# Kernel tuning notes

Measured on AMD Instinct MI355X. Metric: run time of the kernel, lower is better.

The kernel has to match this reference:

```python
import jax, jax.numpy as jnp
import numpy as np


def _l2n(v, eps=1e-12):
    return v / (jnp.linalg.norm(v) + eps)


def _sn(W, u):
    # Spectral normalization with one power-iteration step.
    # W: [Cin, Cout] (1x1 conv kernel flattened), u: [Cin] persistent vector.
    v = _l2n(W.T @ u)            # [Cout]
    u_new = _l2n(W @ v)          # [Cin]
    v = jax.lax.stop_gradient(v)
    u_new = jax.lax.stop_gradient(u_new)
    sigma = u_new @ (W @ v)      # scalar, grads flow through W only
    return W / sigma


def _conv1x1(x, W, b, u):
    # x: [B,H,W,Cin], spectrally-normalized 1x1 conv == GEMM over channels
    return jnp.einsum('bhwc,cd->bhwd', x, _sn(W, u)) + b


def setup_inputs() -> dict:
    key = jax.random.key(0)
    ks = jax.random.split(key, 14)
    B, H, W, C = 8, 64, 64, 256
    Cq = C // 8  # 32
    s = lambda fan_in: 1.0 / np.sqrt(fan_in)
    return {
        'x':  jax.random.normal(ks[0], (B, H, W, C), jnp.float32),
        'Wf': jax.random.normal(ks[1], (C, Cq), jnp.float32) * s(C),
        'bf': jnp.zeros((Cq,), jnp.float32),
        'uf': jax.random.normal(ks[2], (C,), jnp.float32),
        'Wg': jax.random.normal(ks[3], (C, Cq), jnp.float32) * s(C),
        'bg': jnp.zeros((Cq,), jnp.float32),
        'ug': jax.random.normal(ks[4], (C,), jnp.float32),
        'Wh': jax.random.normal(ks[5], (C, C), jnp.float32) * s(C),
        'bh': jnp.zeros((C,), jnp.float32),
        'uh': jax.random.normal(ks[6], (C,), jnp.float32),
        'Wc': jax.random.normal(ks[7], (C, C), jnp.float32) * s(C),
        'bc': jnp.zeros((C,), jnp.float32),
        'uc': jax.random.normal(ks[8], (C,), jnp.float32),
        'gamma': jnp.float32(0.7),  # nonzero so attention branch contributes
    }


def reference(x, Wf, bf, uf, Wg, bg, ug, Wh, bh, uh, Wc, bc, uc, gamma):
    B, H, W, C = x.shape
    N = H * W
    flat = lambda t: t.reshape(B, N, t.shape[-1])
    f = flat(_conv1x1(x, Wf, bf, uf))   # [B,N,C/8] keys
    g = flat(_conv1x1(x, Wg, bg, ug))   # [B,N,C/8] queries
    h = flat(_conv1x1(x, Wh, bh, uh))   # [B,N,C]   values
    s = jnp.einsum('bqd,bkd->bqk', g, f)          # [B,N,N]
    beta = jax.nn.softmax(s, axis=-1)
    o = jnp.einsum('bqk,bkc->bqc', beta, h)       # [B,N,C]
    o = o.reshape(B, H, W, C)
    o = _conv1x1(o, Wc, bc, uc)
    return gamma * o + x
```

## Files before the change

kernel.cpp:

```cpp
#include <hip/hip_runtime.h>

typedef unsigned short ushort_t;
typedef __attribute__((ext_vector_type(8))) __bf16 bf16x8;
typedef __attribute__((ext_vector_type(4))) float f32x4;
typedef __attribute__((ext_vector_type(4))) ushort_t ushort4_t;

__device__ inline ushort_t f2bf(float f){
  __bf16 h = (__bf16)f;
  union { __bf16 h; ushort_t u; } v; v.h = h;
  return v.u;
}

__device__ inline f32x4 mfma16(bf16x8 a, bf16x8 b, f32x4 c){
  return __builtin_amdgcn_mfma_f32_16x16x32_bf16(a, b, c, 0, 0, 0);
}

#define GLDS16(gsrc, ldst) \
  __builtin_amdgcn_global_load_lds((const __attribute__((address_space(1))) unsigned int*)(gsrc), \
                                   (__attribute__((address_space(3))) unsigned int*)(ldst), 16, 0, 0)

__global__ void sigma_kernel(const float* __restrict__ Wf, const float* __restrict__ uf,
                             const float* __restrict__ Wg, const float* __restrict__ ug,
                             const float* __restrict__ Wh, const float* __restrict__ uh,
                             const float* __restrict__ Wc, const float* __restrict__ uc,
                             float* __restrict__ inv_sigma){
  int w = blockIdx.x, t = threadIdx.x;
  const float *W, *u; int Cout;
  if      (w == 0){ W = Wf; u = uf; Cout = 32; }
  else if (w == 1){ W = Wg; u = ug; Cout = 32; }
  else if (w == 2){ W = Wh; u = uh; Cout = 256; }
  else            { W = Wc; u = uc; Cout = 256; }
  __shared__ float su[256], sv[256], red[256];
  su[t] = u[t];
  __syncthreads();
  float v = 0.f;
  if (t < Cout){
    for (int i = 0; i < 256; ++i) v += W[i*Cout + t] * su[i];
  }
  red[t] = (t < Cout) ? v*v : 0.f;
  __syncthreads();
  for (int s = 128; s > 0; s >>= 1){ if (t < s) red[t] += red[t+s]; __syncthreads(); }
  float nv = sqrtf(red[0]) + 1e-12f;
  __syncthreads();
  if (t < Cout) sv[t] = v / nv;
  __syncthreads();
  float wv = 0.f;
  for (int d = 0; d < Cout; ++d) wv += W[t*Cout + d] * sv[d];
  __syncthreads();
  red[t] = wv * wv;
  __syncthreads();
  for (int s = 128; s > 0; s >>= 1){ if (t < s) red[t] += red[t+s]; __syncthreads(); }
  if (t == 0){
    float ss2 = red[0];
    float sig = ss2 / (sqrtf(ss2) + 1e-12f);
    inv_sigma[w] = 1.0f / sig;
  }
}

__global__ void prep_weights(const float* __restrict__ Wf, const float* __restrict__ Wg,
                             const float* __restrict__ Wh, const float* __restrict__ Wc,
                             const float* __restrict__ inv_sigma,
                             ushort_t* __restrict__ WallT, ushort_t* __restrict__ WcT){
  int idx = blockIdx.x * 256 + threadIdx.x;
  if (idx < 81920){
    int c = idx >> 8, k = idx & 255;
    float val, is;
    if (c < 32)      { val = Wf[k*32  + c      ]; is = inv_sigma[0]; }
    else if (c < 64) { val = Wg[k*32  + (c-32) ]; is = inv_sigma[1]; }
    else             { val = Wh[k*256 + (c-64) ]; is = inv_sigma[2]; }
    WallT[idx] = f2bf(val * is);
  } else {
    int j = idx - 81920; int c = j >> 8, k = j & 255;
    WcT[j] = f2bf(Wc[k*256 + c] * inv_sigma[3]);
  }
}

__global__ __launch_bounds__(256) void fgh_kernel(
    const float* __restrict__ x, const ushort_t* __restrict__ WallT,
    const float* __restrict__ bf, const float* __restrict__ bg, const float* __restrict__ bh,
    ushort_t* __restrict__ fO, ushort_t* __restrict__ gO, ushort_t* __restrict__ hT){
  __shared__ __attribute__((aligned(16))) char ldsX[4][16384];
  int t = threadIdx.x;
  int wv = t >> 6, l = t & 63, lrow = l & 15, lgrp = l >> 4;
  long r0 = (long)blockIdx.x * 64 + wv * 16;
  char* ldsW = ldsX[wv];
#pragma unroll
  for (int rloc = 0; rloc < 16; ++rloc){
    const char* src = (const char*)(x + (r0 + rloc)*256)
                    + ((l*16) ^ ((rloc & 7) << 4));
    GLDS16(src, ldsW + rloc*1024);
  }
  asm volatile("s_waitcnt vmcnt(0)" ::: "memory");
  const char* xrow = ldsW + lrow*1024;
  int swzX = (lrow & 7) << 4;
  f32x4 acc[20];
#pragma unroll
  for (int i = 0; i < 20; ++i) acc[i] = f32x4{0.f,0.f,0.f,0.f};
#pragma unroll
  for (int ks = 0; ks < 8; ++ks){
    int bb = ks*128 + lgrp*32;
    f32x4 xa = *(const f32x4*)(xrow + ( bb       ^ swzX));
    f32x4 xb = *(const f32x4*)(xrow + ((bb + 16) ^ swzX));
    union { __bf16 h[8]; bf16x8 v; } A;
#pragma unroll
    for (int j = 0; j < 4; ++j){ A.h[j] = (__bf16)xa[j]; A.h[4+j] = (__bf16)xb[j]; }
    int kk = ks*32 + lgrp*8;
#pragma unroll
    for (int ct = 0; ct < 20; ++ct){
      bf16x8 bbv = *(const bf16x8*)(WallT + (ct*16 + lrow)*256 + kk);
      acc[ct] = mfma16(A.v, bbv, acc[ct]);
    }
  }
#pragma unroll
  for (int ct = 0; ct < 20; ++ct){
    int col = ct*16 + lrow;
    long rowb = r0 + lgrp*4;
    if (col < 32){
      float bv = bf[col];
#pragma unroll
      for (int rg = 0; rg < 4; ++rg) fO[(rowb+rg)*32 + col] = f2bf(acc[ct][rg] + bv);
    } else if (col < 64){
      float bv = bg[col-32];
#pragma unroll
      for (int rg = 0; rg < 4; ++rg)
        gO[(rowb+rg)*32 + (col-32)] = f2bf((acc[ct][rg] + bv) * 1.44269504f);
    } else {
      int hc = col - 64;
      float bv = bh[hc];
      long bb2 = rowb >> 12, n = rowb & 4095;
      int k6 = (int)(n & 63);
      int s6 = (k6 & 32) | (((k6 >> 2) & 3) << 3) | (((k6 >> 4) & 1) << 2) | (k6 & 3);
      long pos = (n & ~63L) | (long)s6;
      ushort4_t pk;
#pragma unroll
      for (int rg = 0; rg < 4; ++rg) pk[rg] = f2bf(acc[ct][rg] + bv);
      *(ushort4_t*)(hT + (bb2*256 + hc)*4096 + pos) = pk;
    }
  }
}

__global__ __launch_bounds__(256, 2) void attn_kernel(
    const ushort_t* __restrict__ fI, const ushort_t* __restrict__ gI,
    const ushort_t* __restrict__ hT,
    ushort_t* __restrict__ oP, float* __restrict__ mP, float* __restrict__ liP){
  __shared__ ushort_t ldsV[256*64];
  int bid = blockIdx.x, t = threadIdx.x;
  int b = bid & 7, rest = bid >> 3, qt = rest >> 1, kh = rest & 1;
  int wv = t >> 6, l = t & 63, lrow = l & 15, lgrp = l >> 4;
  int q0 = qt*128 + wv*32;
  long key_base = (long)kh * 2048;
  const ushort_t* gB = gI + ((long)b*4096 + q0)*32;
  bf16x8 qa0 = *(const bf16x8*)(gB + lrow*32 + lgrp*8);
  bf16x8 qa1 = *(const bf16x8*)(gB + (16 + lrow)*32 + lgrp*8);
  const ushort_t* hB = hT + (long)b*256*4096;
  const ushort_t* kp = fI + (long)b*4096*32 + key_base*32 + lrow*32 + lgrp*8;
  const ushort_t* vsrc = hB + (long)(wv*64 + (l>>3))*4096 + key_base
                            + (((l & 7) ^ (l >> 3)) << 3);
  ushort_t* vdst = ldsV + wv*4096;
  f32x4 o0[16], o1[16];
#pragma unroll
  for (int i = 0; i < 16; ++i){ o0[i] = f32x4{0.f,0.f,0.f,0.f}; o1[i] = f32x4{0.f,0.f,0.f,0.f}; }
  float m0 = -1e30f, m1 = -1e30f, li0 = 0.f, li1 = 0.f;
  int swzR = (lrow & 7) << 3;
  for (int kt = 0; kt < 32; ++kt){
    __syncthreads();
    bf16x8 kb0 = *(const bf16x8*)(kp);
    bf16x8 kb1 = *(const bf16x8*)(kp + 512);
    bf16x8 kb2 = *(const bf16x8*)(kp + 1024);
    bf16x8 kb3 = *(const bf16x8*)(kp + 1536);
    kp += 2048;
    const ushort_t* vs = vsrc + kt*64;
#pragma unroll
    for (int i = 0; i < 8; ++i)
      GLDS16(vs + i*32768, vdst + i*512);
    f32x4 s00 = mfma16(kb0, qa0, f32x4{0.f,0.f,0.f,0.f});
    f32x4 s01 = mfma16(kb1, qa0, f32x4{0.f,0.f,0.f,0.f});
    f32x4 s02 = mfma16(kb2, qa0, f32x4{0.f,0.f,0.f,0.f});
    f32x4 s03 = mfma16(kb3, qa0, f32x4{0.f,0.f,0.f,0.f});
    f32x4 s10 = mfma16(kb0, qa1, f32x4{0.f,0.f,0.f,0.f});
    f32x4 s11 = mfma16(kb1, qa1, f32x4{0.f,0.f,0.f,0.f});
    f32x4 s12 = mfma16(kb2, qa1, f32x4{0.f,0.f,0.f,0.f});
    f32x4 s13 = mfma16(kb3, qa1, f32x4{0.f,0.f,0.f,0.f});
    float tm0 = -1e30f, tm1 = -1e30f;
#pragma unroll
    for (int rg = 0; rg < 4; ++rg){
      tm0 = fmaxf(tm0, fmaxf(fmaxf(s00[rg], s01[rg]), fmaxf(s02[rg], s03[rg])));
      tm1 = fmaxf(tm1, fmaxf(fmaxf(s10[rg], s11[rg]), fmaxf(s12[rg], s13[rg])));
    }
    tm0 = fmaxf(tm0, __shfl_xor(tm0, 16)); tm0 = fmaxf(tm0, __shfl_xor(tm0, 32));
    tm1 = fmaxf(tm1, __shfl_xor(tm1, 16)); tm1 = fmaxf(tm1, __shfl_xor(tm1, 32));
    if (__any((tm0 > m0 + 8.f) || (tm1 > m1 + 8.f))){
      float mn0 = fmaxf(m0, tm0), mn1 = fmaxf(m1, tm1);
      float sc0 = exp2f(m0 - mn0), sc1 = exp2f(m1 - mn1);
      m0 = mn0; m1 = mn1; li0 *= sc0; li1 *= sc1;
#pragma unroll
      for (int ct = 0; ct < 16; ++ct)
#pragma unroll
        for (int rg = 0; rg < 4; ++rg){ o0[ct][rg] *= sc0; o1[ct][rg] *= sc1; }
    }
    union { __bf16 h[8]; bf16x8 v; } pf00, pf01, pf10, pf11;
#pragma unroll
    for (int rg = 0; rg < 4; ++rg){
      float a0 = exp2f(s00[rg] - m0), a1 = exp2f(s01[rg] - m0);
      float a2 = exp2f(s02[rg] - m0), a3 = exp2f(s03[rg] - m0);
      li0 += (a0 + a1) + (a2 + a3);
      pf00.h[rg] = (__bf16)a0; pf00.h[4+rg] = (__bf16)a1;
      pf01.h[rg] = (__bf16)a2; pf01.h[4+rg] = (__bf16)a3;
      float c0 = exp2f(s10[rg] - m1), c1 = exp2f(s11[rg] - m1);
      float c2 = exp2f(s12[rg] - m1), c3 = exp2f(s13[rg] - m1);
      li1 += (c0 + c1) + (c2 + c3);
      pf10.h[rg] = (__bf16)c0; pf10.h[4+rg] = (__bf16)c1;
      pf11.h[rg] = (__bf16)c2; pf11.h[4+rg] = (__bf16)c3;
    }
    asm volatile("s_waitcnt vmcnt(0)" ::: "memory");
    __syncthreads();
    __builtin_amdgcn_s_setprio(1);
#pragma unroll
    for (int ct = 0; ct < 16; ++ct){
      int base = (ct*16 + lrow) << 6;
      bf16x8 vb0 = *(const bf16x8*)(ldsV + base + (( (lgrp << 3))      ^ swzR));
      bf16x8 vb1 = *(const bf16x8*)(ldsV + base + ((32 + (lgrp << 3)) ^ swzR));
      o0[ct] = mfma16(vb0, pf00.v, o0[ct]);
      o0[ct] = mfma16(vb1, pf01.v, o0[ct]);
      o1[ct] = mfma16(vb0, pf10.v, o1[ct]);
      o1[ct] = mfma16(vb1, pf11.v, o1[ct]);
    }
    __builtin_amdgcn_s_setprio(0);
  }
  li0 += __shfl_xor(li0, 16); li0 += __shfl_xor(li0, 32);
  li1 += __shfl_xor(li1, 16); li1 += __shfl_xor(li1, 32);
  long rbase = (long)b*4096 + q0;
  ushort_t* Ob = oP + ((long)kh*32768 + rbase)*256;
#pragma unroll
  for (int ct = 0; ct < 16; ++ct){
    ushort4_t pk0, pk1;
#pragma unroll
    for (int rg = 0; rg < 4; ++rg){ pk0[rg] = f2bf(o0[ct][rg]); pk1[rg] = f2bf(o1[ct][rg]); }
    *(ushort4_t*)(Ob + (long)lrow*256      + ct*16 + lgrp*4) = pk0;
    *(ushort4_t*)(Ob + (long)(16+lrow)*256 + ct*16 + lgrp*4) = pk1;
  }
  if (l < 16){
    mP [kh*32768 + rbase + lrow]      = m0;
    liP[kh*32768 + rbase + lrow]      = li0;
    mP [kh*32768 + rbase + 16 + lrow] = m1;
    liP[kh*32768 + rbase + 16 + lrow] = li1;
  }
}

__global__ __launch_bounds__(256) void out_kernel(
    const ushort_t* __restrict__ oP, const float* __restrict__ mP,
    const float* __restrict__ liP, const ushort_t* __restrict__ WcT,
    const float* __restrict__ bc, const float* __restrict__ x,
    const float* __restrict__ gamma, float* __restrict__ out){
  __shared__ __attribute__((aligned(16))) char ldsO[4][16384];
  int t = threadIdx.x;
  int wv = t >> 6, l = t & 63, lrow = l & 15, lgrp = l >> 4;
  long r0 = (long)blockIdx.x * 64 + wv * 16;
  char* ldsW = ldsO[wv];
#pragma unroll
  for (int i = 0; i < 8; ++i){
    int rloc = 2*i + (l >> 5);
    int soff = ((l & 31)*16) ^ ((rloc & 7) << 4);
    GLDS16((const char*)(oP + (r0 + rloc)*256) + soff,            ldsW + i*1024);
    GLDS16((const char*)(oP + (32768L + r0 + rloc)*256) + soff,   ldsW + 8192 + i*1024);
  }
  long r = r0 + lrow;
  float m1 = mP[r],  m2 = mP[32768 + r];
  float li1 = liP[r], li2 = liP[32768 + r];
  float mm  = fmaxf(m1, m2);
  float sc1 = exp2f(m1 - mm), sc2 = exp2f(m2 - mm);
  float inv = 1.0f / (li1*sc1 + li2*sc2);
  float w1 = sc1 * inv, w2 = sc2 * inv;
  asm volatile("s_waitcnt vmcnt(0)" ::: "memory");
  const char* orow = ldsW + lrow*512;
  int swzO = (lrow & 7) << 4;
  f32x4 acc[16];
#pragma unroll
  for (int i = 0; i < 16; ++i) acc[i] = f32x4{0.f,0.f,0.f,0.f};
#pragma unroll
  for (int ks = 0; ks < 8; ++ks){
    int bb = (ks*64 + lgrp*16) ^ swzO;
    bf16x8 a1 = *(const bf16x8*)(orow + bb);
    bf16x8 a2 = *(const bf16x8*)(orow + 8192 + bb);
    union { __bf16 h[8]; bf16x8 v; } A;
#pragma unroll
    for (int j = 0; j < 8; ++j)
      A.h[j] = (__bf16)((float)a1[j]*w1 + (float)a2[j]*w2);
    int kk = ks*32 + lgrp*8;
#pragma unroll
    for (int ct = 0; ct < 16; ++ct){
      bf16x8 bbv = *(const bf16x8*)(WcT + (ct*16 + lrow)*256 + kk);
      acc[ct] = mfma16(A.v, bbv, acc[ct]);
    }
  }
  float gm = gamma[0];
#pragma unroll
  for (int ct = 0; ct < 16; ++ct){
    int col = ct*16 + lrow;
    float bv = bc[col];
#pragma unroll
    for (int rg = 0; rg < 4; ++rg){
      long row = r0 + lgrp*4 + rg;
      out[row*256 + col] = gm*(acc[ct][rg] + bv) + x[row*256 + col];
    }
  }
}

extern "C" void kernel_launch(void* const* d_in, const int* in_sizes, int n_in,
                              void* d_out, int out_size, void* d_ws, size_t ws_size,
                              hipStream_t stream){
  (void)in_sizes; (void)n_in; (void)out_size; (void)ws_size;
  const float* x  = (const float*)d_in[0];
  const float* Wf = (const float*)d_in[1];
  const float* bf = (const float*)d_in[2];
  const float* uf = (const float*)d_in[3];
  const float* Wg = (const float*)d_in[4];
  const float* bg = (const float*)d_in[5];
  const float* ug = (const float*)d_in[6];
  const float* Wh = (const float*)d_in[7];
  const float* bh = (const float*)d_in[8];
  const float* uh = (const float*)d_in[9];
  const float* Wc = (const float*)d_in[10];
  const float* bc = (const float*)d_in[11];
  const float* uc = (const float*)d_in[12];
  const float* gamma = (const float*)d_in[13];
  float* out = (float*)d_out;

  char* w = (char*)d_ws;
  float*    inv_sigma = (float*)w;
  ushort_t* WallT = (ushort_t*)(w + 256);
  ushort_t* WcT   = (ushort_t*)(w + 164096);
  ushort_t* fW    = (ushort_t*)(w + 295168);
  ushort_t* gW    = (ushort_t*)(w + 2392320);
  ushort_t* hTW   = (ushort_t*)(w + 4489472);
  ushort_t* oPW   = (ushort_t*)(w + 21266688);
  float*    mPW   = (float*)   (w + 54821120);
  float*    liPW  = (float*)   (w + 55083264);

  hipLaunchKernelGGL(sigma_kernel, dim3(4),    dim3(256), 0, stream,
                     Wf, uf, Wg, ug, Wh, uh, Wc, uc, inv_sigma);
  hipLaunchKernelGGL(prep_weights, dim3(576),  dim3(256), 0, stream,
                     Wf, Wg, Wh, Wc, inv_sigma, WallT, WcT);
  hipLaunchKernelGGL(fgh_kernel,   dim3(512),  dim3(256), 0, stream,
                     x, WallT, bf, bg, bh, fW, gW, hTW);
  hipLaunchKernelGGL(attn_kernel,  dim3(512),  dim3(256), 0, stream,
                     fW, gW, hTW, oPW, mPW, liPW);
  hipLaunchKernelGGL(out_kernel,   dim3(512),  dim3(256), 0, stream,
                     oPW, mPW, liPW, WcT, bc, x, gamma, out);
}
```

Measured before the change: 206.2 us.

## Double-buffer V tiles in LDS to prefetch next key block during compute

Replaces the single LDS buffer for V with two ping-pong buffers. The next key tile's V load (global-to-LDS) and K register loads are issued before the current tile's QK, softmax and PV work, so the memory latency can overlap with MFMA compute instead of being waited on every iteration. LDS use per block doubles to 64 KB, which may limit the two-blocks-per-CU occupancy target, and K prefetch registers add pressure.

```diff
diff --git a/kernel.cpp b/kernel.cpp
--- a/kernel.cpp
+++ b/kernel.cpp
@@ -139,11 +139,64 @@
   }
 }
 
+#define QK_SM_PV(KB0,KB1,KB2,KB3,BUF)                                          \
+  {                                                                            \
+    f32x4 z = f32x4{0.f,0.f,0.f,0.f};                                          \
+    f32x4 s00 = mfma16(KB0, qa0, z), s01 = mfma16(KB1, qa0, z);                \
+    f32x4 s02 = mfma16(KB2, qa0, z), s03 = mfma16(KB3, qa0, z);                \
+    f32x4 s10 = mfma16(KB0, qa1, z), s11 = mfma16(KB1, qa1, z);                \
+    f32x4 s12 = mfma16(KB2, qa1, z), s13 = mfma16(KB3, qa1, z);                \
+    float tm0 = -1e30f, tm1 = -1e30f;                                          \
+    _Pragma("unroll")                                                          \
+    for (int rg = 0; rg < 4; ++rg){                                            \
+      tm0 = fmaxf(tm0, fmaxf(fmaxf(s00[rg], s01[rg]), fmaxf(s02[rg], s03[rg])));\
+      tm1 = fmaxf(tm1, fmaxf(fmaxf(s10[rg], s11[rg]), fmaxf(s12[rg], s13[rg])));\
+    }                                                                          \
+    tm0 = fmaxf(tm0, __shfl_xor(tm0, 16)); tm0 = fmaxf(tm0, __shfl_xor(tm0, 32));\
+    tm1 = fmaxf(tm1, __shfl_xor(tm1, 16)); tm1 = fmaxf(tm1, __shfl_xor(tm1, 32));\
+    if (__any((tm0 > m0 + 8.f) || (tm1 > m1 + 8.f))){                          \
+      float mn0 = fmaxf(m0, tm0), mn1 = fmaxf(m1, tm1);                        \
+      float sc0 = exp2f(m0 - mn0), sc1 = exp2f(m1 - mn1);                      \
+      m0 = mn0; m1 = mn1; li0 *= sc0; li1 *= sc1;                              \
+      _Pragma("unroll")                                                        \
+      for (int ct = 0; ct < 16; ++ct)                                          \
+        _Pragma("unroll")                                                      \
+        for (int rg = 0; rg < 4; ++rg){ o0[ct][rg] *= sc0; o1[ct][rg] *= sc1; }\
+    }                                                                          \
+    union { __bf16 h[8]; bf16x8 v; } pf00, pf01, pf10, pf11;                   \
+    _Pragma("unroll")                                                          \
+    for (int rg = 0; rg < 4; ++rg){                                            \
+      float a0 = exp2f(s00[rg] - m0), a1 = exp2f(s01[rg] - m0);                \
+      float a2 = exp2f(s02[rg] - m0), a3 = exp2f(s03[rg] - m0);                \
+      li0 += (a0 + a1) + (a2 + a3);                                            \
+      pf00.h[rg] = (__bf16)a0; pf00.h[4+rg] = (__bf16)a1;                      \
+      pf01.h[rg] = (__bf16)a2; pf01.h[4+rg] = (__bf16)a3;                      \
+      float c0 = exp2f(s10[rg] - m1), c1 = exp2f(s11[rg] - m1);                \
+      float c2 = exp2f(s12[rg] - m1), c3 = exp2f(s13[rg] - m1);                \
+      li1 += (c0 + c1) + (c2 + c3);                                            \
+      pf10.h[rg] = (__bf16)c0; pf10.h[4+rg] = (__bf16)c1;                      \
+      pf11.h[rg] = (__bf16)c2; pf11.h[4+rg] = (__bf16)c3;                      \
+    }                                                                          \
+    __builtin_amdgcn_s_setprio(1);                                             \
+    _Pragma("unroll")                                                          \
+    for (int ct = 0; ct < 16; ++ct){                                           \
+      int base = (ct*16 + lrow) << 6;                                          \
+      bf16x8 vb0 = *(const bf16x8*)((BUF) + base + (( (lgrp << 3))      ^ swzR));\
+      bf16x8 vb1 = *(const bf16x8*)((BUF) + base + ((32 + (lgrp << 3)) ^ swzR));\
+      o0[ct] = mfma16(vb0, pf00.v, o0[ct]);                                    \
+      o0[ct] = mfma16(vb1, pf01.v, o0[ct]);                                    \
+      o1[ct] = mfma16(vb0, pf10.v, o1[ct]);                                    \
+      o1[ct] = mfma16(vb1, pf11.v, o1[ct]);                                    \
+    }                                                                          \
+    __builtin_amdgcn_s_setprio(0);                                             \
+  }
+
 __global__ __launch_bounds__(256, 2) void attn_kernel(
     const ushort_t* __restrict__ fI, const ushort_t* __restrict__ gI,
     const ushort_t* __restrict__ hT,
     ushort_t* __restrict__ oP, float* __restrict__ mP, float* __restrict__ liP){
-  __shared__ ushort_t ldsV[256*64];
+  __shared__ ushort_t ldsVA[256*64];
+  __shared__ ushort_t ldsVB[256*64];
   int bid = blockIdx.x, t = threadIdx.x;
   int b = bid & 7, rest = bid >> 3, qt = rest >> 1, kh = rest & 1;
   int wv = t >> 6, l = t & 63, lrow = l & 15, lgrp = l >> 4;
@@ -156,76 +209,49 @@
   const ushort_t* kp = fI + (long)b*4096*32 + key_base*32 + lrow*32 + lgrp*8;
   const ushort_t* vsrc = hB + (long)(wv*64 + (l>>3))*4096 + key_base
                             + (((l & 7) ^ (l >> 3)) << 3);
-  ushort_t* vdst = ldsV + wv*4096;
   f32x4 o0[16], o1[16];
 #pragma unroll
   for (int i = 0; i < 16; ++i){ o0[i] = f32x4{0.f,0.f,0.f,0.f}; o1[i] = f32x4{0.f,0.f,0.f,0.f}; }
   float m0 = -1e30f, m1 = -1e30f, li0 = 0.f, li1 = 0.f;
   int swzR = (lrow & 7) << 3;
-  for (int kt = 0; kt < 32; ++kt){
-    __syncthreads();
-    bf16x8 kb0 = *(const bf16x8*)(kp);
-    bf16x8 kb1 = *(const bf16x8*)(kp + 512);
-    bf16x8 kb2 = *(const bf16x8*)(kp + 1024);
-    bf16x8 kb3 = *(const bf16x8*)(kp + 1536);
-    kp += 2048;
-    const ushort_t* vs = vsrc + kt*64;
-#pragma unroll
-    for (int i = 0; i < 8; ++i)
-      GLDS16(vs + i*32768, vdst + i*512);
-    f32x4 s00 = mfma16(kb0, qa0, f32x4{0.f,0.f,0.f,0.f});
-    f32x4 s01 = mfma16(kb1, qa0, f32x4{0.f,0.f,0.f,0.f});
-    f32x4 s02 = mfma16(kb2, qa0, f32x4{0.f,0.f,0.f,0.f});
-    f32x4 s03 = mfma16(kb3, qa0, f32x4{0.f,0.f,0.f,0.f});
-    f32x4 s10 = mfma16(kb0, qa1, f32x4{0.f,0.f,0.f,0.f});
-    f32x4 s11 = mfma16(kb1, qa1, f32x4{0.f,0.f,0.f,0.f});
-    f32x4 s12 = mfma16(kb2, qa1, f32x4{0.f,0.f,0.f,0.f});
-    f32x4 s13 = mfma16(kb3, qa1, f32x4{0.f,0.f,0.f,0.f});
-    float tm0 = -1e30f, tm1 = -1e30f;
-#pragma unroll
-    for (int rg = 0; rg < 4; ++rg){
-      tm0 = fmaxf(tm0, fmaxf(fmaxf(s00[rg], s01[rg]), fmaxf(s02[rg], s03[rg])));
-      tm1 = fmaxf(tm1, fmaxf(fmaxf(s10[rg], s11[rg]), fmaxf(s12[rg], s13[rg])));
-    }
-    tm0 = fmaxf(tm0, __shfl_xor(tm0, 16)); tm0 = fmaxf(tm0, __shfl_xor(tm0, 32));
-    tm1 = fmaxf(tm1, __shfl_xor(tm1, 16)); tm1 = fmaxf(tm1, __shfl_xor(tm1, 32));
-    if (__any((tm0 > m0 + 8.f) || (tm1 > m1 + 8.f))){
-      float mn0 = fmaxf(m0, tm0), mn1 = fmaxf(m1, tm1);
-      float sc0 = exp2f(m0 - mn0), sc1 = exp2f(m1 - mn1);
-      m0 = mn0; m1 = mn1; li0 *= sc0; li1 *= sc1;
-#pragma unroll
-      for (int ct = 0; ct < 16; ++ct)
-#pragma unroll
-        for (int rg = 0; rg < 4; ++rg){ o0[ct][rg] *= sc0; o1[ct][rg] *= sc1; }
-    }
-    union { __bf16 h[8]; bf16x8 v; } pf00, pf01, pf10, pf11;
-#pragma unroll
-    for (int rg = 0; rg < 4; ++rg){
-      float a0 = exp2f(s00[rg] - m0), a1 = exp2f(s01[rg] - m0);
-      float a2 = exp2f(s02[rg] - m0), a3 = exp2f(s03[rg] - m0);
-      li0 += (a0 + a1) + (a2 + a3);
-      pf00.h[rg] = (__bf16)a0; pf00.h[4+rg] = (__bf16)a1;
-      pf01.h[rg] = (__bf16)a2; pf01.h[4+rg] = (__bf16)a3;
-      float c0 = exp2f(s10[rg] - m1), c1 = exp2f(s11[rg] - m1);
-      float c2 = exp2f(s12[rg] - m1), c3 = exp2f(s13[rg] - m1);
-      li1 += (c0 + c1) + (c2 + c3);
-      pf10.h[rg] = (__bf16)c0; pf10.h[4+rg] = (__bf16)c1;
-      pf11.h[rg] = (__bf16)c2; pf11.h[4+rg] = (__bf16)c3;
-    }
+  int vofs = wv*4096;
+#pragma unroll
+  for (int i = 0; i < 8; ++i) GLDS16(vsrc + i*32768, ldsVA + vofs + i*512);
+  bf16x8 kA0 = *(const bf16x8*)(kp);
+  bf16x8 kA1 = *(const bf16x8*)(kp + 512);
+  bf16x8 kA2 = *(const bf16x8*)(kp + 1024);
+  bf16x8 kA3 = *(const bf16x8*)(kp + 1536);
+  kp += 2048;
+  asm volatile("s_waitcnt vmcnt(0)" ::: "memory");
+  __syncthreads();
+  bf16x8 kB0, kB1, kB2, kB3;
+  for (int it = 0; it < 16; ++it){
+    {
+      const ushort_t* vs = vsrc + (2*it + 1)*64;
+#pragma unroll
+      for (int i = 0; i < 8; ++i) GLDS16(vs + i*32768, ldsVB + vofs + i*512);
+      kB0 = *(const bf16x8*)(kp);
+      kB1 = *(const bf16x8*)(kp + 512);
+      kB2 = *(const bf16x8*)(kp + 1024);
+      kB3 = *(const bf16x8*)(kp + 1536);
+      kp += 2048;
+    }
+    QK_SM_PV(kA0, kA1, kA2, kA3, ldsVA)
     asm volatile("s_waitcnt vmcnt(0)" ::: "memory");
     __syncthreads();
-    __builtin_amdgcn_s_setprio(1);
-#pragma unroll
-    for (int ct = 0; ct < 16; ++ct){
-      int base = (ct*16 + lrow) << 6;
-      bf16x8 vb0 = *(const bf16x8*)(ldsV + base + (( (lgrp << 3))      ^ swzR));
-      bf16x8 vb1 = *(const bf16x8*)(ldsV + base + ((32 + (lgrp << 3)) ^ swzR));
-      o0[ct] = mfma16(vb0, pf00.v, o0[ct]);
-      o0[ct] = mfma16(vb1, pf01.v, o0[ct]);
-      o1[ct] = mfma16(vb0, pf10.v, o1[ct]);
-      o1[ct] = mfma16(vb1, pf11.v, o1[ct]);
-    }
-    __builtin_amdgcn_s_setprio(0);
+    if (it < 15){
+      const ushort_t* vs = vsrc + (2*it + 2)*64;
+#pragma unroll
+      for (int i = 0; i < 8; ++i) GLDS16(vs + i*32768, ldsVA + vofs + i*512);
+      kA0 = *(const bf16x8*)(kp);
+      kA1 = *(const bf16x8*)(kp + 512);
+      kA2 = *(const bf16x8*)(kp + 1024);
+      kA3 = *(const bf16x8*)(kp + 1536);
+      kp += 2048;
+    }
+    QK_SM_PV(kB0, kB1, kB2, kB3, ldsVB)
+    asm volatile("s_waitcnt vmcnt(0)" ::: "memory");
+    __syncthreads();
   }
   li0 += __shfl_xor(li0, 16); li0 += __shfl_xor(li0, 32);
   li1 += __shfl_xor(li1, 16); li1 += __shfl_xor(li1, 32);
```

After: 208.5 us. Within noise of the previous version (+1.1%).

## Split attention waves over query and channel halves to halve V LDS reads

Applied to the files above, without the earlier changes.

Reassigns the four waves in the attention block from 32 queries × 256 value channels each to 64 queries × 128 channels each (two query halves × two channel halves). Each V fragment read from LDS now feeds four query tiles instead of two, halving LDS read traffic per MFMA in the PV product. The cost is that each pair of waves sharing a query half computes QK scores and exponentials redundantly, doubling that work per wave. The key tile is processed in two 32-key halves with an online max rescale that also rescales the first half's probabilities.

```diff
diff --git a/kernel.cpp b/kernel.cpp
--- a/kernel.cpp
+++ b/kernel.cpp
@@ -145,105 +145,134 @@
     ushort_t* __restrict__ oP, float* __restrict__ mP, float* __restrict__ liP){
   __shared__ ushort_t ldsV[256*64];
   int bid = blockIdx.x, t = threadIdx.x;
-  int b = bid & 7, rest = bid >> 3, qt = rest >> 1, kh = rest & 1;
+  int b = bid & 7, rest = bid >> 3, qg = rest >> 1, kh = rest & 1;
   int wv = t >> 6, l = t & 63, lrow = l & 15, lgrp = l >> 4;
-  int q0 = qt*128 + wv*32;
+  int qh = wv >> 1, dh = wv & 1;
+  int q0 = qg*128 + qh*64;
   long key_base = (long)kh * 2048;
   const ushort_t* gB = gI + ((long)b*4096 + q0)*32;
-  bf16x8 qa0 = *(const bf16x8*)(gB + lrow*32 + lgrp*8);
-  bf16x8 qa1 = *(const bf16x8*)(gB + (16 + lrow)*32 + lgrp*8);
+  bf16x8 qa[4];
+#pragma unroll
+  for (int qt = 0; qt < 4; ++qt)
+    qa[qt] = *(const bf16x8*)(gB + (qt*16 + lrow)*32 + lgrp*8);
   const ushort_t* hB = hT + (long)b*256*4096;
   const ushort_t* kp = fI + (long)b*4096*32 + key_base*32 + lrow*32 + lgrp*8;
   const ushort_t* vsrc = hB + (long)(wv*64 + (l>>3))*4096 + key_base
                             + (((l & 7) ^ (l >> 3)) << 3);
   ushort_t* vdst = ldsV + wv*4096;
-  f32x4 o0[16], o1[16];
-#pragma unroll
-  for (int i = 0; i < 16; ++i){ o0[i] = f32x4{0.f,0.f,0.f,0.f}; o1[i] = f32x4{0.f,0.f,0.f,0.f}; }
-  float m0 = -1e30f, m1 = -1e30f, li0 = 0.f, li1 = 0.f;
+  f32x4 o[8][4];
+#pragma unroll
+  for (int ct = 0; ct < 8; ++ct)
+#pragma unroll
+    for (int qt = 0; qt < 4; ++qt) o[ct][qt] = f32x4{0.f,0.f,0.f,0.f};
+  float m[4]  = {-1e30f,-1e30f,-1e30f,-1e30f};
+  float li[4] = {0.f,0.f,0.f,0.f};
   int swzR = (lrow & 7) << 3;
+  int vrow0 = dh << 7;
   for (int kt = 0; kt < 32; ++kt){
     __syncthreads();
-    bf16x8 kb0 = *(const bf16x8*)(kp);
-    bf16x8 kb1 = *(const bf16x8*)(kp + 512);
-    bf16x8 kb2 = *(const bf16x8*)(kp + 1024);
-    bf16x8 kb3 = *(const bf16x8*)(kp + 1536);
+    const ushort_t* vs = vsrc + kt*64;
+#pragma unroll
+    for (int i = 0; i < 8; ++i) GLDS16(vs + i*32768, vdst + i*512);
+    bf16x8 pfA[4], pfB[4];
+#pragma unroll
+    for (int h = 0; h < 2; ++h){
+      bf16x8 kb0 = *(const bf16x8*)(kp + h*1024);
+      bf16x8 kb1 = *(const bf16x8*)(kp + h*1024 + 512);
+      f32x4 z = f32x4{0.f,0.f,0.f,0.f};
+      f32x4 s0[4], s1[4];
+#pragma unroll
+      for (int qt = 0; qt < 4; ++qt){
+        s0[qt] = mfma16(kb0, qa[qt], z);
+        s1[qt] = mfma16(kb1, qa[qt], z);
+      }
+      float tm[4]; int viol = 0;
+#pragma unroll
+      for (int qt = 0; qt < 4; ++qt){
+        float v0 = fmaxf(fmaxf(fmaxf(s0[qt][0], s0[qt][1]), fmaxf(s0[qt][2], s0[qt][3])),
+                         fmaxf(fmaxf(s1[qt][0], s1[qt][1]), fmaxf(s1[qt][2], s1[qt][3])));
+        tm[qt] = v0;
+        viol |= (v0 > m[qt] + 8.f) ? 1 : 0;
+      }
+      if (__any(viol)){
+#pragma unroll
+        for (int qt = 0; qt < 4; ++qt){
+          float tq = tm[qt];
+          tq = fmaxf(tq, __shfl_xor(tq, 16));
+          tq = fmaxf(tq, __shfl_xor(tq, 32));
+          float mn = fmaxf(m[qt], tq);
+          float sc = exp2f(m[qt] - mn);
+          m[qt] = mn; li[qt] *= sc;
+#pragma unroll
+          for (int ct = 0; ct < 8; ++ct)
+#pragma unroll
+            for (int rg = 0; rg < 4; ++rg) o[ct][qt][rg] *= sc;
+          if (h == 1){
+            union { __bf16 hh[8]; bf16x8 v; } u; u.v = pfA[qt];
+#pragma unroll
+            for (int j = 0; j < 8; ++j) u.hh[j] = (__bf16)((float)u.hh[j] * sc);
+            pfA[qt] = u.v;
+          }
+        }
+      }
+#pragma unroll
+      for (int qt = 0; qt < 4; ++qt){
+        union { __bf16 hh[8]; bf16x8 v; } pf;
+        float p0 = exp2f(s0[qt][0] - m[qt]);
+        float p1 = exp2f(s0[qt][1] - m[qt]);
+        float p2 = exp2f(s0[qt][2] - m[qt]);
+        float p3 = exp2f(s0[qt][3] - m[qt]);
+        float p4 = exp2f(s1[qt][0] - m[qt]);
+        float p5 = exp2f(s1[qt][1] - m[qt]);
+        float p6 = exp2f(s1[qt][2] - m[qt]);
+        float p7 = exp2f(s1[qt][3] - m[qt]);
+        li[qt] += ((p0 + p1) + (p2 + p3)) + ((p4 + p5) + (p6 + p7));
+        pf.hh[0] = (__bf16)p0; pf.hh[1] = (__bf16)p1;
+        pf.hh[2] = (__bf16)p2; pf.hh[3] = (__bf16)p3;
+        pf.hh[4] = (__bf16)p4; pf.hh[5] = (__bf16)p5;
+        pf.hh[6] = (__bf16)p6; pf.hh[7] = (__bf16)p7;
+        if (h == 0) pfA[qt] = pf.v; else pfB[qt] = pf.v;
+      }
+    }
     kp += 2048;
-    const ushort_t* vs = vsrc + kt*64;
-#pragma unroll
-    for (int i = 0; i < 8; ++i)
-      GLDS16(vs + i*32768, vdst + i*512);
-    f32x4 s00 = mfma16(kb0, qa0, f32x4{0.f,0.f,0.f,0.f});
-    f32x4 s01 = mfma16(kb1, qa0, f32x4{0.f,0.f,0.f,0.f});
-    f32x4 s02 = mfma16(kb2, qa0, f32x4{0.f,0.f,0.f,0.f});
-    f32x4 s03 = mfma16(kb3, qa0, f32x4{0.f,0.f,0.f,0.f});
-    f32x4 s10 = mfma16(kb0, qa1, f32x4{0.f,0.f,0.f,0.f});
-    f32x4 s11 = mfma16(kb1, qa1, f32x4{0.f,0.f,0.f,0.f});
-    f32x4 s12 = mfma16(kb2, qa1, f32x4{0.f,0.f,0.f,0.f});
-    f32x4 s13 = mfma16(kb3, qa1, f32x4{0.f,0.f,0.f,0.f});
-    float tm0 = -1e30f, tm1 = -1e30f;
-#pragma unroll
-    for (int rg = 0; rg < 4; ++rg){
-      tm0 = fmaxf(tm0, fmaxf(fmaxf(s00[rg], s01[rg]), fmaxf(s02[rg], s03[rg])));
-      tm1 = fmaxf(tm1, fmaxf(fmaxf(s10[rg], s11[rg]), fmaxf(s12[rg], s13[rg])));
-    }
-    tm0 = fmaxf(tm0, __shfl_xor(tm0, 16)); tm0 = fmaxf(tm0, __shfl_xor(tm0, 32));
-    tm1 = fmaxf(tm1, __shfl_xor(tm1, 16)); tm1 = fmaxf(tm1, __shfl_xor(tm1, 32));
-    if (__any((tm0 > m0 + 8.f) || (tm1 > m1 + 8.f))){
-      float mn0 = fmaxf(m0, tm0), mn1 = fmaxf(m1, tm1);
-      float sc0 = exp2f(m0 - mn0), sc1 = exp2f(m1 - mn1);
-      m0 = mn0; m1 = mn1; li0 *= sc0; li1 *= sc1;
-#pragma unroll
-      for (int ct = 0; ct < 16; ++ct)
-#pragma unroll
-        for (int rg = 0; rg < 4; ++rg){ o0[ct][rg] *= sc0; o1[ct][rg] *= sc1; }
-    }
-    union { __bf16 h[8]; bf16x8 v; } pf00, pf01, pf10, pf11;
-#pragma unroll
-    for (int rg = 0; rg < 4; ++rg){
-      float a0 = exp2f(s00[rg] - m0), a1 = exp2f(s01[rg] - m0);
-      float a2 = exp2f(s02[rg] - m0), a3 = exp2f(s03[rg] - m0);
-      li0 += (a0 + a1) + (a2 + a3);
-      pf00.h[rg] = (__bf16)a0; pf00.h[4+rg] = (__bf16)a1;
-      pf01.h[rg] = (__bf16)a2; pf01.h[4+rg] = (__bf16)a3;
-      float c0 = exp2f(s10[rg] - m1), c1 = exp2f(s11[rg] - m1);
-      float c2 = exp2f(s12[rg] - m1), c3 = exp2f(s13[rg] - m1);
-      li1 += (c0 + c1) + (c2 + c3);
-      pf10.h[rg] = (__bf16)c0; pf10.h[4+rg] = (__bf16)c1;
-      pf11.h[rg] = (__bf16)c2; pf11.h[4+rg] = (__bf16)c3;
-    }
     asm volatile("s_waitcnt vmcnt(0)" ::: "memory");
     __syncthreads();
     __builtin_amdgcn_s_setprio(1);
 #pragma unroll
-    for (int ct = 0; ct < 16; ++ct){
-      int base = (ct*16 + lrow) << 6;
+    for (int ct = 0; ct < 8; ++ct){
+      int base = (vrow0 + ct*16 + lrow) << 6;
       bf16x8 vb0 = *(const bf16x8*)(ldsV + base + (( (lgrp << 3))      ^ swzR));
       bf16x8 vb1 = *(const bf16x8*)(ldsV + base + ((32 + (lgrp << 3)) ^ swzR));
-      o0[ct] = mfma16(vb0, pf00.v, o0[ct]);
-      o0[ct] = mfma16(vb1, pf01.v, o0[ct]);
-      o1[ct] = mfma16(vb0, pf10.v, o1[ct]);
-      o1[ct] = mfma16(vb1, pf11.v, o1[ct]);
+#pragma unroll
+      for (int qt = 0; qt < 4; ++qt){
+        o[ct][qt] = mfma16(vb0, pfA[qt], o[ct][qt]);
+        o[ct][qt] = mfma16(vb1, pfB[qt], o[ct][qt]);
+      }
     }
     __builtin_amdgcn_s_setprio(0);
   }
-  li0 += __shfl_xor(li0, 16); li0 += __shfl_xor(li0, 32);
-  li1 += __shfl_xor(li1, 16); li1 += __shfl_xor(li1, 32);
+#pragma unroll
+  for (int qt = 0; qt < 4; ++qt){
+    li[qt] += __shfl_xor(li[qt], 16);
+    li[qt] += __shfl_xor(li[qt], 32);
+  }
   long rbase = (long)b*4096 + q0;
   ushort_t* Ob = oP + ((long)kh*32768 + rbase)*256;
 #pragma unroll
-  for (int ct = 0; ct < 16; ++ct){
-    ushort4_t pk0, pk1;
-#pragma unroll
-    for (int rg = 0; rg < 4; ++rg){ pk0[rg] = f2bf(o0[ct][rg]); pk1[rg] = f2bf(o1[ct][rg]); }
-    *(ushort4_t*)(Ob + (long)lrow*256      + ct*16 + lgrp*4) = pk0;
-    *(ushort4_t*)(Ob + (long)(16+lrow)*256 + ct*16 + lgrp*4) = pk1;
-  }
-  if (l < 16){
-    mP [kh*32768 + rbase + lrow]      = m0;
-    liP[kh*32768 + rbase + lrow]      = li0;
-    mP [kh*32768 + rbase + 16 + lrow] = m1;
-    liP[kh*32768 + rbase + 16 + lrow] = li1;
+  for (int ct = 0; ct < 8; ++ct)
+#pragma unroll
+    for (int qt = 0; qt < 4; ++qt){
+      ushort4_t pk;
+#pragma unroll
+      for (int rg = 0; rg < 4; ++rg) pk[rg] = f2bf(o[ct][qt][rg]);
+      *(ushort4_t*)(Ob + (long)(qt*16 + lrow)*256 + vrow0 + ct*16 + lgrp*4) = pk;
+    }
+  if (dh == 0 && l < 16){
+#pragma unroll
+    for (int qt = 0; qt < 4; ++qt){
+      mP [kh*32768 + rbase + qt*16 + lrow] = m[qt];
+      liP[kh*32768 + rbase + qt*16 + lrow] = li[qt];
+    }
   }
 }
 
```

Measured after the change: 257.6 us. 1.25x slower.
